# Kernel optimization log

Measured on AMD Instinct MI355X. Metric: run time of the kernel, lower is better.

Reference implementation:

```python
import jax, jax.numpy as jnp
import numpy as np

EMBED_DIM = 512
N_HEADS = 8
HEAD_DIM = EMBED_DIM // N_HEADS
B, N = 4, 2048


def setup_inputs() -> dict:
    key = jax.random.key(0)
    ks = jax.random.split(key, 5)
    x = jax.random.normal(ks[0], (B, N, EMBED_DIM), dtype=jnp.float32)
    # torch Linear weights are (out, in); init scale ~ 1/sqrt(in)
    s = 1.0 / np.sqrt(EMBED_DIM)
    WQ = jax.random.uniform(ks[1], (EMBED_DIM, EMBED_DIM), jnp.float32, -s, s)
    WK = jax.random.uniform(ks[2], (EMBED_DIM, EMBED_DIM), jnp.float32, -s, s)
    WV = jax.random.uniform(ks[3], (EMBED_DIM, EMBED_DIM), jnp.float32, -s, s)
    WO = jax.random.uniform(ks[4], (EMBED_DIM, EMBED_DIM), jnp.float32, -s, s)
    mask = jnp.tril(jnp.ones((N, N), dtype=jnp.int32))  # causal mask
    return {"x": x, "WQ": WQ, "WK": WK, "WV": WV, "WO": WO, "mask": mask}


def reference(x, WQ, WK, WV, WO, mask):
    scale = HEAD_DIM ** -0.5
    # Linear: y = x @ W.T ; then split heads -> (B, H, N, Dh)
    def proj(W):
        y = jnp.einsum('bnd,ed->bne', x, W)
        return y.reshape(B, N, N_HEADS, HEAD_DIM).transpose(0, 2, 1, 3)
    Q, K, V = proj(WQ), proj(WK), proj(WV)
    scores = jnp.einsum('bhnd,bhmd->bhnm', Q, K) * scale  # (B,H,N,N)
    scores = jnp.where(mask[None, None, :, :] == 0, -jnp.inf, scores)
    attn = jax.nn.softmax(scores, axis=-1)
    # dropout is identity in eval mode
    out = jnp.einsum('bhnm,bhmd->bhnd', attn, V)
    out = out.transpose(0, 2, 1, 3).reshape(B, N, EMBED_DIM)
    return jnp.einsum('bne,de->bnd', out, WO)
```

## Files before the change

kernel.cpp:

```cpp
#include <hip/hip_runtime.h>
#include <hip/hip_bf16.h>

#define B_  4
#define N_  2048
#define E_  512
#define H_  8
#define DH_ 64
#define M_  (B_ * N_)

typedef __attribute__((ext_vector_type(8))) short bq8;
typedef __attribute__((ext_vector_type(4))) float f32x4;

#define QSCALE_ (0.125f * 1.44269504f)

static __device__ __forceinline__ unsigned short f2bf(float f) {
    unsigned u = __float_as_uint(f);
    unsigned r = (u + 0x7fffu + ((u >> 16) & 1u)) >> 16;
    return (unsigned short)r;
}

static __device__ __forceinline__ unsigned cvtpk_bf16(float lo, float hi) {
    unsigned r;
    asm("v_cvt_pk_bf16_f32 %0, %1, %2" : "=v"(r) : "v"(lo), "v"(hi));
    return r;
}

static __device__ __forceinline__ void gld_lds16(const unsigned short* g,
                                                 unsigned short* l)
{
    __builtin_amdgcn_global_load_lds(
        (const __attribute__((address_space(1))) void*)g,
        (__attribute__((address_space(3))) void*)l,
        16, 0, 0);
}

static __device__ __forceinline__ void cvt16(const void* src, unsigned short* dst,
                                             int base, bool isBf)
{
    if (isBf) {
        const uint4* s = (const uint4*)((const unsigned short*)src + base);
        uint4 a = s[0], b = s[1];
        *(uint4*)(dst + base)     = a;
        *(uint4*)(dst + base + 8) = b;
    } else {
        const float* s = (const float*)src + base;
        unsigned short tmp[16];
        #pragma unroll
        for (int c = 0; c < 16; c += 4) {
            const float4 v = *(const float4*)(s + c);
            tmp[c + 0] = f2bf(v.x); tmp[c + 1] = f2bf(v.y);
            tmp[c + 2] = f2bf(v.z); tmp[c + 3] = f2bf(v.w);
        }
        *(uint4*)(dst + base)     = *(uint4*)&tmp[0];
        *(uint4*)(dst + base + 8) = *(uint4*)&tmp[8];
    }
}

__global__ __launch_bounds__(256)
void cvt_all(const void* __restrict__ sx,
             const void* __restrict__ s0, const void* __restrict__ s1,
             const void* __restrict__ s2, const void* __restrict__ s3,
             unsigned short* __restrict__ dx,
             unsigned short* __restrict__ d0, unsigned short* __restrict__ d1,
             unsigned short* __restrict__ d2, unsigned short* __restrict__ d3,
             int* __restrict__ dflag)
{
    __shared__ int wtot[4];
    const int bid = blockIdx.x;
    const int t   = threadIdx.x;
    const void* s;
    unsigned short* d;
    int base;
    if (bid < 1024) {
        s = sx; d = dx;
        base = bid * 4096 + t * 16;
    } else {
        const int wb = bid - 1024;
        const int wi = wb >> 6;
        s = (wi == 0) ? s0 : (wi == 1) ? s1 : (wi == 2) ? s2 : s3;
        d = (wi == 0) ? d0 : (wi == 1) ? d1 : (wi == 2) ? d2 : d3;
        base = (wb & 63) * 4096 + t * 16;
    }

    const unsigned* sw = (const unsigned*)s;
    int cnt = 0;
    #pragma unroll
    for (int i = 0; i < 4; ++i) {
        const unsigned w = sw[t * 4 + i];
        const unsigned elo = (w >> 7) & 0xffu;
        const unsigned ehi = (w >> 23) & 0xffu;
        cnt += (elo >= 100u && elo <= 150u && ehi >= 100u && ehi <= 150u) ? 1 : 0;
    }
    cnt += __shfl_xor(cnt, 1);  cnt += __shfl_xor(cnt, 2);
    cnt += __shfl_xor(cnt, 4);  cnt += __shfl_xor(cnt, 8);
    cnt += __shfl_xor(cnt, 16); cnt += __shfl_xor(cnt, 32);
    if ((t & 63) == 0) wtot[t >> 6] = cnt;
    __syncthreads();
    const int total = wtot[0] + wtot[1] + wtot[2] + wtot[3];
    const bool isBf = (total >= 512);
    if (bid == 0 && t == 0) dflag[0] = isBf ? 1 : 0;

    cvt16(s, d, base, isBf);
}

template<int BN>
__global__ __launch_bounds__(256)
void gemm_bf16(const unsigned short* __restrict__ A,
               const unsigned short* __restrict__ W0,
               const unsigned short* __restrict__ W1,
               const unsigned short* __restrict__ W2,
               void* __restrict__ C0, void* __restrict__ C1, void* __restrict__ C2,
               const int* __restrict__ dflag, int cSel)
{
    constexpr int NB = BN / 32;
    __shared__ unsigned short As[2][128 * 32];
    __shared__ unsigned short Bs[2][BN * 32];

    const int extBf = dflag[0];
    const unsigned short* Wv = (blockIdx.z == 0) ? W0 : (blockIdx.z == 1) ? W1 : W2;
    void*                 Cv = (blockIdx.z == 0) ? C0 : (blockIdx.z == 1) ? C1 : C2;
    const int  mode  = (cSel == 1) ? 1 : ((blockIdx.z == 2) ? 2 : 0);
    const bool vswap = (mode == 2);
    const float qs = (cSel == 0 && blockIdx.z == 0) ? QSCALE_ : 1.0f;

    const int t    = threadIdx.x;
    const int w    = t >> 6;
    const int lane = t & 63;
    const int ln   = lane & 15;
    const int qd   = lane >> 4;
    const int wm   = w >> 1;
    const int wn   = w & 1;

    const int m0 = blockIdx.x * 128;
    const int n0 = blockIdx.y * BN;

    const int lr = lane >> 2;
    const int lc = (lane & 3) * 8;
    const unsigned short* gA0 = A + (size_t)(m0 + w * 32 + lr) * E_ + lc;
    const unsigned short* gA1 = gA0 + 16 * E_;
    const int aOff0 = w * 32 * 32;
    const int aOff1 = aOff0 + 16 * 32;

    const unsigned short* gB0;
    const unsigned short* gB1 = nullptr;
    int bOff0, bOff1 = 0;
    if (BN == 128) {
        gB0 = Wv + (size_t)(n0 + w * 32 + lr) * E_ + lc;
        gB1 = gB0 + 16 * E_;
        bOff0 = w * 32 * 32;
        bOff1 = bOff0 + 16 * 32;
    } else {
        gB0 = Wv + (size_t)(n0 + w * 16 + lr) * E_ + lc;
        bOff0 = w * 16 * 32;
    }

    f32x4 acc[4][4];
    #pragma unroll
    for (int i = 0; i < 4; ++i)
        #pragma unroll
        for (int j = 0; j < 4; ++j)
            acc[i][j] = (f32x4){0.f, 0.f, 0.f, 0.f};

    gld_lds16(gA0, &As[0][aOff0]);
    gld_lds16(gA1, &As[0][aOff1]);
    gld_lds16(gB0, &Bs[0][bOff0]);
    if (BN == 128) gld_lds16(gB1, &Bs[0][bOff1]);

    int cur = 0;
    for (int k0 = 0; k0 < E_; k0 += 32) {
        __syncthreads();
        const int nxt = cur ^ 1;
        if (k0 + 32 < E_) {
            gld_lds16(gA0 + k0 + 32, &As[nxt][aOff0]);
            gld_lds16(gA1 + k0 + 32, &As[nxt][aOff1]);
            gld_lds16(gB0 + k0 + 32, &Bs[nxt][bOff0]);
            if (BN == 128) gld_lds16(gB1 + k0 + 32, &Bs[nxt][bOff1]);
        }

        bq8 afr[4], bfr[NB];
        #pragma unroll
        for (int i = 0; i < 4; ++i)
            afr[i] = *(const bq8*)&As[cur][(wm * 64 + i * 16 + ln) * 32 + qd * 8];
        #pragma unroll
        for (int j = 0; j < NB; ++j)
            bfr[j] = *(const bq8*)&Bs[cur][(wn * (BN / 2) + j * 16 + ln) * 32 + qd * 8];

        if (vswap) {
            #pragma unroll
            for (int i = 0; i < 4; ++i)
                #pragma unroll
                for (int j = 0; j < NB; ++j)
                    acc[i][j] = __builtin_amdgcn_mfma_f32_16x16x32_bf16(afr[i], bfr[j], acc[i][j], 0, 0, 0);
        } else {
            #pragma unroll
            for (int i = 0; i < NB; ++i)
                #pragma unroll
                for (int j = 0; j < 4; ++j)
                    acc[i][j] = __builtin_amdgcn_mfma_f32_16x16x32_bf16(bfr[i], afr[j], acc[i][j], 0, 0, 0);
        }
        cur = nxt;
    }

    if (mode == 2) {
        unsigned short* C = (unsigned short*)Cv;
        const int colBase = n0 + wn * 64;
        const int hh = colBase >> 6;
        #pragma unroll
        for (int i = 0; i < 4; ++i) {
            const int token = m0 + wm * 64 + i * 16 + qd * 4;
            const int bb = token >> 11;
            const int nn = token & 2047;
            #pragma unroll
            for (int j = 0; j < 4; ++j) {
                const int d = j * 16 + ln;
                ushort4 o4;
                o4.x = f2bf(acc[i][j][0]);
                o4.y = f2bf(acc[i][j][1]);
                o4.z = f2bf(acc[i][j][2]);
                o4.w = f2bf(acc[i][j][3]);
                *(ushort4*)(C + ((size_t)(bb * H_ + hh) * 64 + d) * N_ + nn) = o4;
            }
        }
    } else if (mode == 0 || extBf) {
        unsigned short* C = (unsigned short*)Cv;
        #pragma unroll
        for (int i = 0; i < NB; ++i) {
            const int n = n0 + wn * (BN / 2) + i * 16 + qd * 4;
            #pragma unroll
            for (int j = 0; j < 4; ++j) {
                const int m = m0 + wm * 64 + j * 16 + ln;
                ushort4 o4;
                o4.x = f2bf(acc[i][j][0] * qs);
                o4.y = f2bf(acc[i][j][1] * qs);
                o4.z = f2bf(acc[i][j][2] * qs);
                o4.w = f2bf(acc[i][j][3] * qs);
                *(ushort4*)(C + (size_t)m * E_ + n) = o4;
            }
        }
    } else {
        float* C = (float*)Cv;
        #pragma unroll
        for (int i = 0; i < NB; ++i) {
            const int n = n0 + wn * (BN / 2) + i * 16 + qd * 4;
            #pragma unroll
            for (int j = 0; j < 4; ++j) {
                const int m = m0 + wm * 64 + j * 16 + ln;
                *(f32x4*)(C + (size_t)m * E_ + n) = acc[i][j];
            }
        }
    }
}

__global__ __launch_bounds__(256)
void attn_causal(const unsigned short* __restrict__ Q,
                 const unsigned short* __restrict__ K,
                 const unsigned short* __restrict__ VtG,
                 unsigned short* __restrict__ O)
{
    __shared__ unsigned short Ks[128 * 72];
    __shared__ unsigned short Vs[64 * 136];
    __shared__ unsigned short Pq[64 * 136];

    const int bx  = blockIdx.x;
    const int qlo = bx;
    const int qhi = 31 - bx;
    const int h   = blockIdx.y;
    const int b   = blockIdx.z;
    const int t   = threadIdx.x;
    const int w    = t >> 6;
    const int lane = t & 63;
    const int ln   = lane & 15;
    const int qd   = lane >> 4;

    const int CA = (qlo + 2) >> 1;
    const int CB = (qhi + 2) >> 1;

    const int col0 = h * DH_;
    const size_t rowBase = (size_t)b * N_;
    const unsigned short* Vhead = VtG + (size_t)(b * H_ + h) * 64 * N_;

    const int jbase = qd * 4;
    const int mloc  = w * 16 + ln;
    const int qAg = qlo * 64 + mloc;
    const int qBg = qhi * 64 + mloc;
    const int prow = mloc * 136;

    const unsigned short* Qa = Q + (rowBase + qAg) * E_ + col0 + qd * 8;
    const unsigned short* Qb = Q + (rowBase + qBg) * E_ + col0 + qd * 8;
    const bq8 qfA0 = *(const bq8*)(Qa);
    const bq8 qfA1 = *(const bq8*)(Qa + 32);
    const bq8 qfB0 = *(const bq8*)(Qb);
    const bq8 qfB1 = *(const bq8*)(Qb + 32);

    const int kr = t >> 1;
    const int kc = (t & 1) * 32;
    const int vr = t >> 2;
    const int vc = (t & 3) * 32;
    const unsigned short* gK = K + (rowBase + kr) * E_ + col0 + kc;
    const unsigned short* gV = Vhead + (size_t)vr * N_ + vc;

    float lA = 0.f, lB = 0.f;
    f32x4 oA[4], oB[4];
    #pragma unroll
    for (int dt = 0; dt < 4; ++dt) {
        oA[dt] = (f32x4){0.f, 0.f, 0.f, 0.f};
        oB[dt] = (f32x4){0.f, 0.f, 0.f, 0.f};
    }

    uint4 kR0, kR1, kR2, kR3, vR0, vR1, vR2, vR3;
    {
        const uint4* ks = (const uint4*)gK;
        kR0 = ks[0]; kR1 = ks[1]; kR2 = ks[2]; kR3 = ks[3];
        const uint4* vs = (const uint4*)gV;
        vR0 = vs[0]; vR1 = vs[1]; vR2 = vs[2]; vR3 = vs[3];
    }

    for (int kt = 0; kt < CB; ++kt) {
        __syncthreads();
        *(uint4*)&Ks[kr * 72 + kc]      = kR0;
        *(uint4*)&Ks[kr * 72 + kc + 8]  = kR1;
        *(uint4*)&Ks[kr * 72 + kc + 16] = kR2;
        *(uint4*)&Ks[kr * 72 + kc + 24] = kR3;
        *(uint4*)&Vs[vr * 136 + vc]      = vR0;
        *(uint4*)&Vs[vr * 136 + vc + 8]  = vR1;
        *(uint4*)&Vs[vr * 136 + vc + 16] = vR2;
        *(uint4*)&Vs[vr * 136 + vc + 24] = vR3;
        __syncthreads();

        if (kt + 1 < CB) {
            const uint4* ks = (const uint4*)(gK + (size_t)(kt + 1) * 128 * E_);
            kR0 = ks[0]; kR1 = ks[1]; kR2 = ks[2]; kR3 = ks[3];
            const uint4* vs = (const uint4*)(gV + (kt + 1) * 128);
            vR0 = vs[0]; vR1 = vs[1]; vR2 = vs[2]; vR3 = vs[3];
        }

        const int gb = kt * 128 + jbase;

        if (kt < CA) {
            const bool diagA = (kt == CA - 1);
            f32x4 sB[8];
            #pragma unroll
            for (int ct = 0; ct < 8; ++ct) {
                const bq8 kf0 = *(const bq8*)&Ks[(ct * 16 + ln) * 72 + qd * 8];
                const bq8 kf1 = *(const bq8*)&Ks[(ct * 16 + ln) * 72 + 32 + qd * 8];
                f32x4 ca = (f32x4){0.f, 0.f, 0.f, 0.f};
                ca = __builtin_amdgcn_mfma_f32_16x16x32_bf16(kf0, qfA0, ca, 0, 0, 0);
                ca = __builtin_amdgcn_mfma_f32_16x16x32_bf16(kf1, qfA1, ca, 0, 0, 0);
                f32x4 c = (f32x4){0.f, 0.f, 0.f, 0.f};
                c = __builtin_amdgcn_mfma_f32_16x16x32_bf16(kf0, qfB0, c, 0, 0, 0);
                c = __builtin_amdgcn_mfma_f32_16x16x32_bf16(kf1, qfB1, c, 0, 0, 0);
                sB[ct] = c;
                float p0 = exp2f(ca[0]);
                float p1 = exp2f(ca[1]);
                float p2 = exp2f(ca[2]);
                float p3 = exp2f(ca[3]);
                if (diagA) {
                    const int kb = gb + ct * 16;
                    if (kb + 0 > qAg) p0 = 0.f;
                    if (kb + 1 > qAg) p1 = 0.f;
                    if (kb + 2 > qAg) p2 = 0.f;
                    if (kb + 3 > qAg) p3 = 0.f;
                }
                lA += (p0 + p1) + (p2 + p3);
                uint2 pk2;
                pk2.x = cvtpk_bf16(p0, p1);
                pk2.y = cvtpk_bf16(p2, p3);
                *(uint2*)&Pq[prow + ct * 16 + jbase] = pk2;
            }
            const bq8 pA0 = *(const bq8*)&Pq[prow + qd * 8];
            const bq8 pA1 = *(const bq8*)&Pq[prow + 32 + qd * 8];
            const bq8 pA2 = *(const bq8*)&Pq[prow + 64 + qd * 8];
            const bq8 pA3 = *(const bq8*)&Pq[prow + 96 + qd * 8];

            #pragma unroll
            for (int ct = 0; ct < 8; ++ct) {
                const float p0 = exp2f(sB[ct][0]);
                const float p1 = exp2f(sB[ct][1]);
                const float p2 = exp2f(sB[ct][2]);
                const float p3 = exp2f(sB[ct][3]);
                lB += (p0 + p1) + (p2 + p3);
                uint2 pk2;
                pk2.x = cvtpk_bf16(p0, p1);
                pk2.y = cvtpk_bf16(p2, p3);
                *(uint2*)&Pq[prow + ct * 16 + jbase] = pk2;
            }
            const bq8 pB0 = *(const bq8*)&Pq[prow + qd * 8];
            const bq8 pB1 = *(const bq8*)&Pq[prow + 32 + qd * 8];
            const bq8 pB2 = *(const bq8*)&Pq[prow + 64 + qd * 8];
            const bq8 pB3 = *(const bq8*)&Pq[prow + 96 + qd * 8];

            __builtin_amdgcn_s_setprio(1);
            #pragma unroll
            for (int dt = 0; dt < 4; ++dt) {
                const int vb = (dt * 16 + ln) * 136;
                const bq8 vf0 = *(const bq8*)&Vs[vb + qd * 8];
                const bq8 vf1 = *(const bq8*)&Vs[vb + 32 + qd * 8];
                const bq8 vf2 = *(const bq8*)&Vs[vb + 64 + qd * 8];
                const bq8 vf3 = *(const bq8*)&Vs[vb + 96 + qd * 8];
                oB[dt] = __builtin_amdgcn_mfma_f32_16x16x32_bf16(vf0, pB0, oB[dt], 0, 0, 0);
                oB[dt] = __builtin_amdgcn_mfma_f32_16x16x32_bf16(vf1, pB1, oB[dt], 0, 0, 0);
                oB[dt] = __builtin_amdgcn_mfma_f32_16x16x32_bf16(vf2, pB2, oB[dt], 0, 0, 0);
                oB[dt] = __builtin_amdgcn_mfma_f32_16x16x32_bf16(vf3, pB3, oB[dt], 0, 0, 0);
                oA[dt] = __builtin_amdgcn_mfma_f32_16x16x32_bf16(vf0, pA0, oA[dt], 0, 0, 0);
                oA[dt] = __builtin_amdgcn_mfma_f32_16x16x32_bf16(vf1, pA1, oA[dt], 0, 0, 0);
                oA[dt] = __builtin_amdgcn_mfma_f32_16x16x32_bf16(vf2, pA2, oA[dt], 0, 0, 0);
                oA[dt] = __builtin_amdgcn_mfma_f32_16x16x32_bf16(vf3, pA3, oA[dt], 0, 0, 0);
            }
            __builtin_amdgcn_s_setprio(0);
        } else {
            const bool diagB = (kt == CB - 1);
            #pragma unroll
            for (int ct = 0; ct < 8; ++ct) {
                const bq8 kf0 = *(const bq8*)&Ks[(ct * 16 + ln) * 72 + qd * 8];
                const bq8 kf1 = *(const bq8*)&Ks[(ct * 16 + ln) * 72 + 32 + qd * 8];
                f32x4 c = (f32x4){0.f, 0.f, 0.f, 0.f};
                c = __builtin_amdgcn_mfma_f32_16x16x32_bf16(kf0, qfB0, c, 0, 0, 0);
                c = __builtin_amdgcn_mfma_f32_16x16x32_bf16(kf1, qfB1, c, 0, 0, 0);
                float p0 = exp2f(c[0]);
                float p1 = exp2f(c[1]);
                float p2 = exp2f(c[2]);
                float p3 = exp2f(c[3]);
                if (diagB) {
                    const int kb = gb + ct * 16;
                    if (kb + 0 > qBg) p0 = 0.f;
                    if (kb + 1 > qBg) p1 = 0.f;
                    if (kb + 2 > qBg) p2 = 0.f;
                    if (kb + 3 > qBg) p3 = 0.f;
                }
                lB += (p0 + p1) + (p2 + p3);
                uint2 pk2;
                pk2.x = cvtpk_bf16(p0, p1);
                pk2.y = cvtpk_bf16(p2, p3);
                *(uint2*)&Pq[prow + ct * 16 + jbase] = pk2;
            }
            const bq8 pB0 = *(const bq8*)&Pq[prow + qd * 8];
            const bq8 pB1 = *(const bq8*)&Pq[prow + 32 + qd * 8];
            const bq8 pB2 = *(const bq8*)&Pq[prow + 64 + qd * 8];
            const bq8 pB3 = *(const bq8*)&Pq[prow + 96 + qd * 8];

            __builtin_amdgcn_s_setprio(1);
            #pragma unroll
            for (int dt = 0; dt < 4; ++dt) {
                const int vb = (dt * 16 + ln) * 136;
                const bq8 vf0 = *(const bq8*)&Vs[vb + qd * 8];
                const bq8 vf1 = *(const bq8*)&Vs[vb + 32 + qd * 8];
                const bq8 vf2 = *(const bq8*)&Vs[vb + 64 + qd * 8];
                const bq8 vf3 = *(const bq8*)&Vs[vb + 96 + qd * 8];
                oB[dt] = __builtin_amdgcn_mfma_f32_16x16x32_bf16(vf0, pB0, oB[dt], 0, 0, 0);
                oB[dt] = __builtin_amdgcn_mfma_f32_16x16x32_bf16(vf1, pB1, oB[dt], 0, 0, 0);
                oB[dt] = __builtin_amdgcn_mfma_f32_16x16x32_bf16(vf2, pB2, oB[dt], 0, 0, 0);
                oB[dt] = __builtin_amdgcn_mfma_f32_16x16x32_bf16(vf3, pB3, oB[dt], 0, 0, 0);
            }
            __builtin_amdgcn_s_setprio(0);
        }
    }

    lA += __shfl_xor(lA, 16); lA += __shfl_xor(lA, 32);
    lB += __shfl_xor(lB, 16); lB += __shfl_xor(lB, 32);
    const float invA = 1.f / lA;
    const float invB = 1.f / lB;

    unsigned short* oAp = O + (rowBase + qlo * 64 + mloc) * E_ + col0 + jbase;
    unsigned short* oBp = O + (rowBase + qhi * 64 + mloc) * E_ + col0 + jbase;
    #pragma unroll
    for (int dt = 0; dt < 4; ++dt) {
        ushort4 a4, b4;
        a4.x = f2bf(oA[dt][0] * invA); a4.y = f2bf(oA[dt][1] * invA);
        a4.z = f2bf(oA[dt][2] * invA); a4.w = f2bf(oA[dt][3] * invA);
        b4.x = f2bf(oB[dt][0] * invB); b4.y = f2bf(oB[dt][1] * invB);
        b4.z = f2bf(oB[dt][2] * invB); b4.w = f2bf(oB[dt][3] * invB);
        *(ushort4*)(oAp + dt * 16) = a4;
        *(ushort4*)(oBp + dt * 16) = b4;
    }
}

extern "C" void kernel_launch(void* const* d_in, const int* in_sizes, int n_in,
                              void* d_out, int out_size, void* d_ws, size_t ws_size,
                              hipStream_t stream)
{
    const void* x  = d_in[0];
    const void* WQ = d_in[1];
    const void* WK = d_in[2];
    const void* WV = d_in[3];
    const void* WO = d_in[4];

    int* dflag = (int*)d_ws;
    unsigned short* xb  = (unsigned short*)((char*)d_ws + 256);
    unsigned short* wqb = xb  + (size_t)M_ * E_;
    unsigned short* wkb = wqb + (size_t)E_ * E_;
    unsigned short* wvb = wkb + (size_t)E_ * E_;
    unsigned short* wob = wvb + (size_t)E_ * E_;
    unsigned short* q   = wob + (size_t)E_ * E_;
    unsigned short* k   = q   + (size_t)M_ * E_;
    unsigned short* v   = k   + (size_t)M_ * E_;
    unsigned short* o   = v   + (size_t)M_ * E_;

    cvt_all<<<1280, 256, 0, stream>>>(x, WQ, WK, WV, WO,
                                      xb, wqb, wkb, wvb, wob, dflag);

    gemm_bf16<128><<<dim3(M_ / 128, E_ / 128, 3), 256, 0, stream>>>(
        xb, wqb, wkb, wvb, q, k, v, dflag, 0);

    attn_causal<<<dim3(16, H_, B_), 256, 0, stream>>>(q, k, v, o);

    gemm_bf16<64><<<dim3(M_ / 128, E_ / 64, 1), 256, 0, stream>>>(
        o, wob, wob, wob, d_out, d_out, d_out, dflag, 1);
}
```

Before: 175.3 us.

## Fuse x fp32-to-bf16 conversion into QKV projection GEMM loads

Drops the separate pass that turned the whole activation tensor x into bf16. The QKV GEMM now reads x directly, as fp32 or bf16, into registers, converts it with packed bf16 instructions, and stores it to a single-buffered LDS tile, with register prefetch of the next K slice. This removes a full read and write of the converted activation and makes the conversion kernel smaller. In exchange, the three QKV GEMMs each read fp32 x, which is twice the bytes, and the GEMM gives up LDS double buffering and direct global-to-LDS loads for a register-staged scheme with two barriers per step.

```diff
diff --git a/kernel.cpp b/kernel.cpp
--- a/kernel.cpp
+++ b/kernel.cpp
@@ -57,29 +57,26 @@
 }
 
 __global__ __launch_bounds__(256)
-void cvt_all(const void* __restrict__ sx,
-             const void* __restrict__ s0, const void* __restrict__ s1,
-             const void* __restrict__ s2, const void* __restrict__ s3,
-             unsigned short* __restrict__ dx,
-             unsigned short* __restrict__ d0, unsigned short* __restrict__ d1,
-             unsigned short* __restrict__ d2, unsigned short* __restrict__ d3,
-             int* __restrict__ dflag)
+void cvt_w(const void* __restrict__ sx,
+           const void* __restrict__ s0, const void* __restrict__ s1,
+           const void* __restrict__ s2, const void* __restrict__ s3,
+           unsigned short* __restrict__ d0, unsigned short* __restrict__ d1,
+           unsigned short* __restrict__ d2, unsigned short* __restrict__ d3,
+           int* __restrict__ dflag)
 {
     __shared__ int wtot[4];
     const int bid = blockIdx.x;
     const int t   = threadIdx.x;
     const void* s;
-    unsigned short* d;
-    int base;
-    if (bid < 1024) {
-        s = sx; d = dx;
-        base = bid * 4096 + t * 16;
+    unsigned short* d = nullptr;
+    int base = 0;
+    if (bid == 256) {
+        s = sx;
     } else {
-        const int wb = bid - 1024;
-        const int wi = wb >> 6;
+        const int wi = bid >> 6;
         s = (wi == 0) ? s0 : (wi == 1) ? s1 : (wi == 2) ? s2 : s3;
         d = (wi == 0) ? d0 : (wi == 1) ? d1 : (wi == 2) ? d2 : d3;
-        base = (wb & 63) * 4096 + t * 16;
+        base = (bid & 63) * 4096 + t * 16;
     }
 
     const unsigned* sw = (const unsigned*)s;
@@ -98,30 +95,33 @@
     __syncthreads();
     const int total = wtot[0] + wtot[1] + wtot[2] + wtot[3];
     const bool isBf = (total >= 512);
-    if (bid == 0 && t == 0) dflag[0] = isBf ? 1 : 0;
-
+
+    if (bid == 256) {
+        if (t == 0) dflag[0] = isBf ? 1 : 0;
+        return;
+    }
     cvt16(s, d, base, isBf);
 }
 
-template<int BN>
 __global__ __launch_bounds__(256)
-void gemm_bf16(const unsigned short* __restrict__ A,
-               const unsigned short* __restrict__ W0,
-               const unsigned short* __restrict__ W1,
-               const unsigned short* __restrict__ W2,
-               void* __restrict__ C0, void* __restrict__ C1, void* __restrict__ C2,
-               const int* __restrict__ dflag, int cSel)
+void gemm_qkv(const void* __restrict__ X,
+              const unsigned short* __restrict__ W0,
+              const unsigned short* __restrict__ W1,
+              const unsigned short* __restrict__ W2,
+              unsigned short* __restrict__ Cq,
+              unsigned short* __restrict__ Ck,
+              unsigned short* __restrict__ Cv,
+              const int* __restrict__ dflag)
 {
-    constexpr int NB = BN / 32;
-    __shared__ unsigned short As[2][128 * 32];
-    __shared__ unsigned short Bs[2][BN * 32];
+    __shared__ unsigned short As[128 * 32];
+    __shared__ unsigned short Bs[128 * 32];
 
     const int extBf = dflag[0];
-    const unsigned short* Wv = (blockIdx.z == 0) ? W0 : (blockIdx.z == 1) ? W1 : W2;
-    void*                 Cv = (blockIdx.z == 0) ? C0 : (blockIdx.z == 1) ? C1 : C2;
-    const int  mode  = (cSel == 1) ? 1 : ((blockIdx.z == 2) ? 2 : 0);
-    const bool vswap = (mode == 2);
-    const float qs = (cSel == 0 && blockIdx.z == 0) ? QSCALE_ : 1.0f;
+    const int z = blockIdx.z;
+    const unsigned short* Wv = (z == 0) ? W0 : (z == 1) ? W1 : W2;
+    unsigned short* C = (z == 0) ? Cq : (z == 1) ? Ck : Cv;
+    const bool vswap = (z == 2);
+    const float qs = (z == 0) ? QSCALE_ : 1.0f;
 
     const int t    = threadIdx.x;
     const int w    = t >> 6;
@@ -132,6 +132,160 @@
     const int wn   = w & 1;
 
     const int m0 = blockIdx.x * 128;
+    const int n0 = blockIdx.y * 128;
+
+    const int lr = lane >> 2;
+    const int lc = (lane & 3) * 8;
+
+    const size_t aRow = (size_t)(m0 + w * 32 + lr) * E_ + lc;
+    const float*          gAf = (const float*)X + aRow;
+    const unsigned short* gAb = (const unsigned short*)X + aRow;
+    const unsigned short* gB0 = Wv + (size_t)(n0 + w * 32 + lr) * E_ + lc;
+    const unsigned short* gB1 = gB0 + 16 * E_;
+
+    unsigned short* wA0 = As + w * 32 * 32 + lane * 8;
+    unsigned short* wA1 = As + w * 32 * 32 + 16 * 32 + lane * 8;
+    unsigned short* wB0 = Bs + w * 32 * 32 + lane * 8;
+    unsigned short* wB1 = Bs + w * 32 * 32 + 16 * 32 + lane * 8;
+
+    f32x4 acc[4][4];
+    #pragma unroll
+    for (int i = 0; i < 4; ++i)
+        #pragma unroll
+        for (int j = 0; j < 4; ++j)
+            acc[i][j] = (f32x4){0.f, 0.f, 0.f, 0.f};
+
+    uint4  aR0, aR1, bR0, bR1;
+    float4 f00, f01, f10, f11;
+
+    if (extBf) {
+        aR0 = *(const uint4*)(gAb);
+        aR1 = *(const uint4*)(gAb + 16 * E_);
+    } else {
+        f00 = *(const float4*)(gAf);
+        f01 = *(const float4*)(gAf + 4);
+        f10 = *(const float4*)(gAf + 16 * E_);
+        f11 = *(const float4*)(gAf + 16 * E_ + 4);
+    }
+    bR0 = *(const uint4*)(gB0);
+    bR1 = *(const uint4*)(gB1);
+
+    for (int k0 = 0; k0 < E_; k0 += 32) {
+        __syncthreads();
+        if (extBf) {
+            *(uint4*)wA0 = aR0;
+            *(uint4*)wA1 = aR1;
+        } else {
+            uint4 c0, c1;
+            c0.x = cvtpk_bf16(f00.x, f00.y); c0.y = cvtpk_bf16(f00.z, f00.w);
+            c0.z = cvtpk_bf16(f01.x, f01.y); c0.w = cvtpk_bf16(f01.z, f01.w);
+            c1.x = cvtpk_bf16(f10.x, f10.y); c1.y = cvtpk_bf16(f10.z, f10.w);
+            c1.z = cvtpk_bf16(f11.x, f11.y); c1.w = cvtpk_bf16(f11.z, f11.w);
+            *(uint4*)wA0 = c0;
+            *(uint4*)wA1 = c1;
+        }
+        *(uint4*)wB0 = bR0;
+        *(uint4*)wB1 = bR1;
+        __syncthreads();
+
+        if (k0 + 32 < E_) {
+            if (extBf) {
+                aR0 = *(const uint4*)(gAb + k0 + 32);
+                aR1 = *(const uint4*)(gAb + 16 * E_ + k0 + 32);
+            } else {
+                f00 = *(const float4*)(gAf + k0 + 32);
+                f01 = *(const float4*)(gAf + k0 + 36);
+                f10 = *(const float4*)(gAf + 16 * E_ + k0 + 32);
+                f11 = *(const float4*)(gAf + 16 * E_ + k0 + 36);
+            }
+            bR0 = *(const uint4*)(gB0 + k0 + 32);
+            bR1 = *(const uint4*)(gB1 + k0 + 32);
+        }
+
+        bq8 afr[4], bfr[4];
+        #pragma unroll
+        for (int i = 0; i < 4; ++i)
+            afr[i] = *(const bq8*)&As[(wm * 64 + i * 16 + ln) * 32 + qd * 8];
+        #pragma unroll
+        for (int j = 0; j < 4; ++j)
+            bfr[j] = *(const bq8*)&Bs[(wn * 64 + j * 16 + ln) * 32 + qd * 8];
+
+        if (vswap) {
+            #pragma unroll
+            for (int i = 0; i < 4; ++i)
+                #pragma unroll
+                for (int j = 0; j < 4; ++j)
+                    acc[i][j] = __builtin_amdgcn_mfma_f32_16x16x32_bf16(afr[i], bfr[j], acc[i][j], 0, 0, 0);
+        } else {
+            #pragma unroll
+            for (int i = 0; i < 4; ++i)
+                #pragma unroll
+                for (int j = 0; j < 4; ++j)
+                    acc[i][j] = __builtin_amdgcn_mfma_f32_16x16x32_bf16(bfr[i], afr[j], acc[i][j], 0, 0, 0);
+        }
+    }
+
+    if (z == 2) {
+        const int colBase = n0 + wn * 64;
+        const int hh = colBase >> 6;
+        #pragma unroll
+        for (int i = 0; i < 4; ++i) {
+            const int token = m0 + wm * 64 + i * 16 + qd * 4;
+            const int bb = token >> 11;
+            const int nn = token & 2047;
+            #pragma unroll
+            for (int j = 0; j < 4; ++j) {
+                const int d = j * 16 + ln;
+                ushort4 o4;
+                o4.x = f2bf(acc[i][j][0]);
+                o4.y = f2bf(acc[i][j][1]);
+                o4.z = f2bf(acc[i][j][2]);
+                o4.w = f2bf(acc[i][j][3]);
+                *(ushort4*)(C + ((size_t)(bb * H_ + hh) * 64 + d) * N_ + nn) = o4;
+            }
+        }
+    } else {
+        #pragma unroll
+        for (int i = 0; i < 4; ++i) {
+            const int n = n0 + wn * 64 + i * 16 + qd * 4;
+            #pragma unroll
+            for (int j = 0; j < 4; ++j) {
+                const int m = m0 + wm * 64 + j * 16 + ln;
+                ushort4 o4;
+                o4.x = f2bf(acc[i][j][0] * qs);
+                o4.y = f2bf(acc[i][j][1] * qs);
+                o4.z = f2bf(acc[i][j][2] * qs);
+                o4.w = f2bf(acc[i][j][3] * qs);
+                *(ushort4*)(C + (size_t)m * E_ + n) = o4;
+            }
+        }
+    }
+}
+
+template<int BN>
+__global__ __launch_bounds__(256)
+void gemm_bf16(const unsigned short* __restrict__ A,
+               const unsigned short* __restrict__ W0,
+               void* __restrict__ C0,
+               const int* __restrict__ dflag)
+{
+    constexpr int NB = BN / 32;
+    __shared__ unsigned short As[2][128 * 32];
+    __shared__ unsigned short Bs[2][BN * 32];
+
+    const int extBf = dflag[0];
+    const unsigned short* Wv = W0;
+    void* Cv = C0;
+
+    const int t    = threadIdx.x;
+    const int w    = t >> 6;
+    const int lane = t & 63;
+    const int ln   = lane & 15;
+    const int qd   = lane >> 4;
+    const int wm   = w >> 1;
+    const int wn   = w & 1;
+
+    const int m0 = blockIdx.x * 128;
     const int n0 = blockIdx.y * BN;
 
     const int lr = lane >> 2;
@@ -141,22 +295,12 @@
     const int aOff0 = w * 32 * 32;
     const int aOff1 = aOff0 + 16 * 32;
 
-    const unsigned short* gB0;
-    const unsigned short* gB1 = nullptr;
-    int bOff0, bOff1 = 0;
-    if (BN == 128) {
-        gB0 = Wv + (size_t)(n0 + w * 32 + lr) * E_ + lc;
-        gB1 = gB0 + 16 * E_;
-        bOff0 = w * 32 * 32;
-        bOff1 = bOff0 + 16 * 32;
-    } else {
-        gB0 = Wv + (size_t)(n0 + w * 16 + lr) * E_ + lc;
-        bOff0 = w * 16 * 32;
-    }
-
-    f32x4 acc[4][4];
+    const unsigned short* gB0 = Wv + (size_t)(n0 + w * 16 + lr) * E_ + lc;
+    const int bOff0 = w * 16 * 32;
+
+    f32x4 acc[NB][4];
     #pragma unroll
-    for (int i = 0; i < 4; ++i)
+    for (int i = 0; i < NB; ++i)
         #pragma unroll
         for (int j = 0; j < 4; ++j)
             acc[i][j] = (f32x4){0.f, 0.f, 0.f, 0.f};
@@ -164,7 +308,6 @@
     gld_lds16(gA0, &As[0][aOff0]);
     gld_lds16(gA1, &As[0][aOff1]);
     gld_lds16(gB0, &Bs[0][bOff0]);
-    if (BN == 128) gld_lds16(gB1, &Bs[0][bOff1]);
 
     int cur = 0;
     for (int k0 = 0; k0 < E_; k0 += 32) {
@@ -174,7 +317,6 @@
             gld_lds16(gA0 + k0 + 32, &As[nxt][aOff0]);
             gld_lds16(gA1 + k0 + 32, &As[nxt][aOff1]);
             gld_lds16(gB0 + k0 + 32, &Bs[nxt][bOff0]);
-            if (BN == 128) gld_lds16(gB1 + k0 + 32, &Bs[nxt][bOff1]);
         }
 
         bq8 afr[4], bfr[NB];
@@ -185,55 +327,27 @@
         for (int j = 0; j < NB; ++j)
             bfr[j] = *(const bq8*)&Bs[cur][(wn * (BN / 2) + j * 16 + ln) * 32 + qd * 8];
 
-        if (vswap) {
-            #pragma unroll
-            for (int i = 0; i < 4; ++i)
-                #pragma unroll
-                for (int j = 0; j < NB; ++j)
-                    acc[i][j] = __builtin_amdgcn_mfma_f32_16x16x32_bf16(afr[i], bfr[j], acc[i][j], 0, 0, 0);
-        } else {
-            #pragma unroll
-            for (int i = 0; i < NB; ++i)
-                #pragma unroll
-                for (int j = 0; j < 4; ++j)
-                    acc[i][j] = __builtin_amdgcn_mfma_f32_16x16x32_bf16(bfr[i], afr[j], acc[i][j], 0, 0, 0);
-        }
+        #pragma unroll
+        for (int i = 0; i < NB; ++i)
+            #pragma unroll
+            for (int j = 0; j < 4; ++j)
+                acc[i][j] = __builtin_amdgcn_mfma_f32_16x16x32_bf16(bfr[i], afr[j], acc[i][j], 0, 0, 0);
         cur = nxt;
     }
 
-    if (mode == 2) {
+    if (extBf) {
         unsigned short* C = (unsigned short*)Cv;
-        const int colBase = n0 + wn * 64;
-        const int hh = colBase >> 6;
-        #pragma unroll
-        for (int i = 0; i < 4; ++i) {
-            const int token = m0 + wm * 64 + i * 16 + qd * 4;
-            const int bb = token >> 11;
-            const int nn = token & 2047;
+        #pragma unroll
+        for (int i = 0; i < NB; ++i) {
+            const int n = n0 + wn * (BN / 2) + i * 16 + qd * 4;
             #pragma unroll
             for (int j = 0; j < 4; ++j) {
-                const int d = j * 16 + ln;
+                const int m = m0 + wm * 64 + j * 16 + ln;
                 ushort4 o4;
                 o4.x = f2bf(acc[i][j][0]);
                 o4.y = f2bf(acc[i][j][1]);
                 o4.z = f2bf(acc[i][j][2]);
                 o4.w = f2bf(acc[i][j][3]);
-                *(ushort4*)(C + ((size_t)(bb * H_ + hh) * 64 + d) * N_ + nn) = o4;
-            }
-        }
-    } else if (mode == 0 || extBf) {
-        unsigned short* C = (unsigned short*)Cv;
-        #pragma unroll
-        for (int i = 0; i < NB; ++i) {
-            const int n = n0 + wn * (BN / 2) + i * 16 + qd * 4;
-            #pragma unroll
-            for (int j = 0; j < 4; ++j) {
-                const int m = m0 + wm * 64 + j * 16 + ln;
-                ushort4 o4;
-                o4.x = f2bf(acc[i][j][0] * qs);
-                o4.y = f2bf(acc[i][j][1] * qs);
-                o4.z = f2bf(acc[i][j][2] * qs);
-                o4.w = f2bf(acc[i][j][3] * qs);
                 *(ushort4*)(C + (size_t)m * E_ + n) = o4;
             }
         }
@@ -495,14 +609,14 @@
     unsigned short* v   = k   + (size_t)M_ * E_;
     unsigned short* o   = v   + (size_t)M_ * E_;
 
-    cvt_all<<<1280, 256, 0, stream>>>(x, WQ, WK, WV, WO,
-                                      xb, wqb, wkb, wvb, wob, dflag);
-
-    gemm_bf16<128><<<dim3(M_ / 128, E_ / 128, 3), 256, 0, stream>>>(
-        xb, wqb, wkb, wvb, q, k, v, dflag, 0);
+    cvt_w<<<257, 256, 0, stream>>>(x, WQ, WK, WV, WO,
+                                   wqb, wkb, wvb, wob, dflag);
+
+    gemm_qkv<<<dim3(M_ / 128, E_ / 128, 3), 256, 0, stream>>>(
+        x, wqb, wkb, wvb, q, k, v, dflag);
 
     attn_causal<<<dim3(16, H_, B_), 256, 0, stream>>>(q, k, v, o);
 
     gemm_bf16<64><<<dim3(M_ / 128, E_ / 64, 1), 256, 0, stream>>>(
-        o, wob, wob, wob, d_out, d_out, d_out, dflag, 1);
-}
+        o, wob, d_out, dflag);
+}
```

Result: slower. 183.1 us (+4.5%).
